# Kernel tuning notes

Hardware: AMD Instinct MI355X
Metric: run time of the kernel (lower is better)

Reference implementation:

```python
import jax, jax.numpy as jnp
import numpy as np
from jax import lax

N = 32768; L = 3000; PER_GRAPH = 64; NUM_GRAPHS = N // PER_GRAPH
DEG = 16; E = N * DEG
HID = 128; OUT3 = 64; NCLS = 2
RED = (L - 100) // 20 + 1   # 146
F_IN = 32 * RED             # 4672
EPS = 1e-5


def setup_inputs() -> dict:
    key = jax.random.key(0)
    ks = jax.random.split(key, 16)
    x = jax.random.normal(ks[0], (N, L), jnp.float32)
    # within-graph random edges: dst stays inside src's graph block
    src = jnp.repeat(jnp.arange(N, dtype=jnp.int32), DEG)
    dst = (src // PER_GRAPH) * PER_GRAPH + jax.random.randint(ks[1], (E,), 0, PER_GRAPH, dtype=jnp.int32)
    edge_index = jnp.stack([src, dst])
    edge_attr = jax.random.uniform(ks[2], (E,), jnp.float32, 0.1, 1.0)
    batch = jnp.repeat(jnp.arange(NUM_GRAPHS, dtype=jnp.int32), PER_GRAPH)
    g = lambda k, sh, fan: jax.random.normal(k, sh, jnp.float32) / np.float32(np.sqrt(fan))
    def bn(k, c):
        k1, k2 = jax.random.split(k)
        return (jnp.ones(c, jnp.float32), jnp.zeros(c, jnp.float32),
                0.1 * jax.random.normal(k1, (c,), jnp.float32),
                jax.random.uniform(k2, (c,), jnp.float32, 0.5, 1.5))
    g1, be1, m1, v1 = bn(ks[7], HID)
    g2, be2, m2, v2 = bn(ks[8], HID)
    g3, be3, m3, v3 = bn(ks[9], OUT3)
    return dict(x=x, edge_index=edge_index, edge_attr=edge_attr, batch=batch,
                conv_w=g(ks[3], (32, 1, 100), 100), conv_b=jnp.zeros(32, jnp.float32),
                W1=g(ks[4], (F_IN, HID), F_IN), b1=jnp.zeros(HID, jnp.float32),
                W2=g(ks[5], (HID, HID), HID), b2=jnp.zeros(HID, jnp.float32),
                W3=g(ks[6], (HID, OUT3), HID), b3=jnp.zeros(OUT3, jnp.float32),
                g1=g1, be1=be1, m1=m1, v1=v1,
                g2=g2, be2=be2, m2=m2, v2=v2,
                g3=g3, be3=be3, m3=m3, v3=v3,
                fc_w=g(ks[10], (OUT3, NCLS), OUT3), fc_b=jnp.zeros(NCLS, jnp.float32))


def _gcn(h, W, b, src, dst, w):
    # PyG GCNConv: linear (no bias) -> sym-normalized weighted aggregation with
    # self-loops (weight 1) -> + bias
    h = h @ W                                               # [N, C]
    deg = jax.ops.segment_sum(w, dst, num_segments=N) + 1.0  # + self-loop
    dinv = jnp.where(deg > 0, lax.rsqrt(deg), 0.0)
    norm = dinv[src] * w * dinv[dst]                         # [E]
    agg = jax.ops.segment_sum(h[src] * norm[:, None], dst, num_segments=N)
    return agg + h * (dinv * dinv)[:, None] + b              # self-loop term


def _bn(x, gamma, beta, mean, var):
    # eval-mode BatchNorm1d with running stats
    return (x - mean) * lax.rsqrt(var + EPS) * gamma + beta


def reference(x, edge_index, edge_attr, batch, conv_w, conv_b, W1, b1, W2, b2, W3, b3,
              g1, be1, m1, v1, g2, be2, m2, v2, g3, be3, m3, v3, fc_w, fc_b):
    src, dst = edge_index[0], edge_index[1]
    # Conv1d feature extractor: [N,1,L] -> [N,32,RED]
    h = lax.conv_general_dilated(x[:, None, :], conv_w, (20,), 'VALID',
                                 dimension_numbers=('NCH', 'OIH', 'NCH'))
    h = jax.nn.relu(h + conv_b[None, :, None]).reshape(N, F_IN)
    h = jax.nn.relu(_bn(_gcn(h, W1, b1, src, dst, edge_attr), g1, be1, m1, v1))
    h = jax.nn.relu(_bn(_gcn(h, W2, b2, src, dst, edge_attr), g2, be2, m2, v2))
    h = jax.nn.relu(_bn(_gcn(h, W3, b3, src, dst, edge_attr), g3, be3, m3, v3))
    # global mean pool over graphs
    sums = jax.ops.segment_sum(h, batch, num_segments=NUM_GRAPHS)
    cnt = jax.ops.segment_sum(jnp.ones((N,), h.dtype), batch, num_segments=NUM_GRAPHS)
    pooled = sums / cnt[:, None]
    return jax.nn.log_softmax(pooled @ fc_w + fc_b, axis=1)
```

## Files before the change

kernel.cpp:

```cpp
#include <hip/hip_runtime.h>
#include <math.h>

typedef float f32x4 __attribute__((ext_vector_type(4)));
typedef short bf16x8 __attribute__((ext_vector_type(8)));

constexpr int N_NODES = 32768;
constexpr int LEN     = 3000;
constexpr int HID     = 128;
constexpr int OUT3    = 64;
constexpr int E_TOT   = 32768*16;
constexpr int PG      = 64;
constexpr int EPG     = 1024;
constexpr int NG      = 512;
constexpr int NCHUNK  = 25;

__device__ __forceinline__ short bf1(float a) {
    unsigned u = __float_as_uint(a);
    return (short)((u + 0x7fff + ((u >> 16) & 1)) >> 16);
}
__device__ __forceinline__ unsigned bfpk2(float a, float b) {
    unsigned ua = __float_as_uint(a); ua = (ua + 0x7fff + ((ua >> 16) & 1)) >> 16;
    unsigned ub = __float_as_uint(b); ub = (ub + 0x7fff + ((ub >> 16) & 1)) >> 16;
    return (ua & 0xffffu) | (ub << 16);
}
__device__ __forceinline__ unsigned long long pk4(float a, float b, float c, float d) {
    return (unsigned long long)bfpk2(a, b) | ((unsigned long long)bfpk2(c, d) << 32);
}

__global__ void pack_w(const float* __restrict__ cw, short* __restrict__ wPf) {
    int tid = blockIdx.x * 256 + threadIdx.x;
    if (tid >= 512) return;
    int lane = tid & 63, i = tid >> 6;
    int Mt = i >> 2, ks = i & 3;
    int c  = Mt * 16 + (lane & 15);
    int kb = ks * 32 + (lane >> 4) * 8;
    bf16x8 v;
    #pragma unroll
    for (int j = 0; j < 8; j++) {
        int k = kb + j;
        v[j] = (k < 100) ? bf1(cw[c * 100 + k]) : (short)0;
    }
    *(bf16x8*)(wPf + tid * 8) = v;
}

__global__ void pack_w1(const float* __restrict__ W1, short* __restrict__ w1f) {
    int tid = blockIdx.x * 256 + threadIdx.x;
    if (tid >= 76800) return;
    int lane  = tid & 63;
    int rest  = tid >> 6;
    int ks    = rest % 6;
    int rest2 = rest / 6;
    int Nt    = rest2 & 7, chunk = rest2 >> 3;
    int r  = chunk * 6 + ks;
    int n  = Nt * 16 + (lane & 15);
    int cb = (lane >> 4) * 8;
    bf16x8 v;
    #pragma unroll
    for (int j = 0; j < 8; j++) {
        int c = cb + j;
        v[j] = (r < 146) ? bf1(W1[(c * 146 + r) * 128 + n]) : (short)0;
    }
    *(bf16x8*)(w1f + tid * 8) = v;
}

__global__ __launch_bounds__(256, 2) void conv_gemm1_mfma(
    const float* __restrict__ x, const short* __restrict__ wPf,
    const float* __restrict__ cbv, const short* __restrict__ w1f,
    float* __restrict__ z)
{
    __shared__ short xs[64 * 264];
    __shared__ short cbuf[64 * 196];

    const int t    = threadIdx.x;
    const int lane = t & 63;
    const int wv   = t >> 6;
    const int l15  = lane & 15;
    const int q    = lane >> 4;
    const int n0   = blockIdx.x * 64;

    bf16x8 wA[8];
    #pragma unroll
    for (int i = 0; i < 8; i++)
        wA[i] = *(const bf16x8*)(wPf + (i * 64 + lane) * 8);
    float cbr[8];
    #pragma unroll
    for (int i = 0; i < 8; i++)
        cbr[i] = cbv[(i >> 2) * 16 + q * 4 + (i & 3)];

    f32x4 acc[4][2];
    #pragma unroll
    for (int a = 0; a < 4; a++) { acc[a][0] = (f32x4)0.0f; acc[a][1] = (f32x4)0.0f; }

    const int NtG0 = wv * 2;
    const int NtC0 = wv * 6;

    #pragma unroll 1
    for (int c = 0; c < NCHUNK; c++) {
        const int r0 = c * 6;
        const int rcount = (146 - r0 < 6) ? (146 - r0) : 6;

        bf16x8 wB[12];
        #pragma unroll
        for (int u = 0; u < 12; u++) {
            int nt2 = u / 6, ks = u - nt2 * 6;
            int flat = (c * 8 + NtG0 + nt2) * 6 + ks;
            wB[u] = *(const bf16x8*)(w1f + (flat * 64 + lane) * 8);
        }

        __syncthreads();
        if (c == 0) {
            for (int u = t; u < 64 * 60; u += 256) {
                int node = u / 60, j = u - node * 60;
                int e = j * 4;
                const float4 vx = *(const float4*)&x[(size_t)(n0 + node) * LEN + e];
                *(unsigned long long*)&xs[node * 264 + (e & 255)] = pk4(vx.x, vx.y, vx.z, vx.w);
            }
        } else {
            const int L = 120 * c + 120;
            for (int u = t; u < 64 * 30; u += 256) {
                int node = u / 30, j = u - node * 30;
                int e  = L + j * 4;
                int ge = (e > 2996) ? 2996 : e;
                const float4 vx = *(const float4*)&x[(size_t)(n0 + node) * LEN + ge];
                *(unsigned long long*)&xs[node * 264 + (e & 255)] = pk4(vx.x, vx.y, vx.z, vx.w);
            }
        }
        __syncthreads();

        for (int ntc = 0; ntc < 6; ntc++) {
            int nn = (NtC0 + ntc) * 16 + l15;
            int m  = nn / 6;
            int rr = nn - m * 6;
            int eb = 20 * (r0 + rr) + q * 8;
            f32x4 ca0 = (f32x4)0.0f, ca1 = (f32x4)0.0f;
            #pragma unroll
            for (int ks = 0; ks < 4; ks++) {
                int e0 = eb + ks * 32;
                bf16x8 bx;
                ((unsigned long long*)&bx)[0] = *(const unsigned long long*)&xs[m * 264 + (e0 & 255)];
                ((unsigned long long*)&bx)[1] = *(const unsigned long long*)&xs[m * 264 + ((e0 + 4) & 255)];
                ca0 = __builtin_amdgcn_mfma_f32_16x16x32_bf16(wA[ks],     bx, ca0, 0, 0, 0);
                ca1 = __builtin_amdgcn_mfma_f32_16x16x32_bf16(wA[4 + ks], bx, ca1, 0, 0, 0);
            }
            const bool valid = (rr < rcount);
            const int wb = m * 196 + rr * 32 + q * 4;
            float v0 = valid ? fmaxf(ca0[0] + cbr[0], 0.f) : 0.f;
            float v1 = valid ? fmaxf(ca0[1] + cbr[1], 0.f) : 0.f;
            float v2 = valid ? fmaxf(ca0[2] + cbr[2], 0.f) : 0.f;
            float v3 = valid ? fmaxf(ca0[3] + cbr[3], 0.f) : 0.f;
            *(unsigned long long*)&cbuf[wb] = pk4(v0, v1, v2, v3);
            v0 = valid ? fmaxf(ca1[0] + cbr[4], 0.f) : 0.f;
            v1 = valid ? fmaxf(ca1[1] + cbr[5], 0.f) : 0.f;
            v2 = valid ? fmaxf(ca1[2] + cbr[6], 0.f) : 0.f;
            v3 = valid ? fmaxf(ca1[3] + cbr[7], 0.f) : 0.f;
            *(unsigned long long*)&cbuf[wb + 16] = pk4(v0, v1, v2, v3);
        }
        __syncthreads();

        #pragma unroll
        for (int ks = 0; ks < 6; ks++) {
            bf16x8 af[4];
            #pragma unroll
            for (int mt = 0; mt < 4; mt++) {
                int ad = (mt * 16 + l15) * 196 + ks * 32 + q * 8;
                ((unsigned long long*)&af[mt])[0] = *(const unsigned long long*)&cbuf[ad];
                ((unsigned long long*)&af[mt])[1] = *(const unsigned long long*)&cbuf[ad + 4];
            }
            #pragma unroll
            for (int mt = 0; mt < 4; mt++) {
                acc[mt][0] = __builtin_amdgcn_mfma_f32_16x16x32_bf16(af[mt], wB[ks],     acc[mt][0], 0, 0, 0);
                acc[mt][1] = __builtin_amdgcn_mfma_f32_16x16x32_bf16(af[mt], wB[6 + ks], acc[mt][1], 0, 0, 0);
            }
        }
    }

    #pragma unroll
    for (int mt = 0; mt < 4; mt++)
        #pragma unroll
        for (int nt2 = 0; nt2 < 2; nt2++)
            #pragma unroll
            for (int reg = 0; reg < 4; reg++) {
                int node = n0 + mt * 16 + q * 4 + reg;
                int f    = (NtG0 + nt2) * 16 + l15;
                z[(size_t)node * HID + f] = acc[mt][nt2][reg];
            }
}

__global__ __launch_bounds__(256) void graph_block(
    const float* __restrict__ z, const int* __restrict__ ei,
    const float* __restrict__ ew,
    const float* __restrict__ b1, const float* __restrict__ g1, const float* __restrict__ be1,
    const float* __restrict__ m1, const float* __restrict__ v1,
    const float* __restrict__ W2,
    const float* __restrict__ b2, const float* __restrict__ g2, const float* __restrict__ be2,
    const float* __restrict__ m2, const float* __restrict__ v2,
    const float* __restrict__ W3,
    const float* __restrict__ b3, const float* __restrict__ g3, const float* __restrict__ be3,
    const float* __restrict__ m3, const float* __restrict__ v3,
    const float* __restrict__ fcw, const float* __restrict__ fcb,
    float* __restrict__ out)
{
    __shared__ float At[64 * 68];
    __shared__ float buf[8704];
    __shared__ float dl[64];
    __shared__ float ps4[256];
    __shared__ float pooled[64];

    const int t  = threadIdx.x;
    const int g  = blockIdx.x;
    const int nb = g * PG;

    for (int i = t; i < 64 * 68; i += 256) At[i] = 0.f;
    if (t < 64) dl[t] = 0.f;
    __syncthreads();
    for (int i = t; i < EPG; i += 256) {
        int e = g * EPG + i;
        atomicAdd(&dl[ei[E_TOT + e] - nb], ew[e]);
    }
    __syncthreads();
    if (t < 64) dl[t] = rsqrtf(dl[t] + 1.0f);
    __syncthreads();
    for (int i = t; i < EPG; i += 256) {
        int e = g * EPG + i;
        int s = ei[e] - nb, d = ei[E_TOT + e] - nb;
        atomicAdd(&At[s * 68 + d], dl[s] * ew[e] * dl[d]);
    }
    if (t < 64) atomicAdd(&At[t * 68 + t], dl[t] * dl[t]);
    for (int i = t; i < 64 * HID; i += 256) buf[i] = z[(size_t)nb * HID + i];
    __syncthreads();

    const int f   = t & 127;
    const int ng  = t >> 7;
    const int n0  = ng * 32;
    const int f3  = t & 63;
    const int ng3 = t >> 6;
    const int n03 = ng3 * 16;

    float hreg[32];

#define LAYER128(BB, GG, BE, MM, VV)                                          \
    {                                                                         \
        float sc = GG[f] * rsqrtf(VV[f] + 1e-5f);                             \
        float mu = MM[f], bt = BE[f], bb = BB[f];                             \
        float a[32];                                                          \
        _Pragma("unroll")                                                     \
        for (int i = 0; i < 32; i++) a[i] = 0.f;                              \
        _Pragma("unroll 2")                                                   \
        for (int s = 0; s < 64; s++) {                                        \
            float zv = buf[s * 128 + f];                                      \
            _Pragma("unroll")                                                 \
            for (int qq = 0; qq < 8; qq++) {                                  \
                float4 a4 = *(const float4*)&At[s * 68 + n0 + qq * 4];        \
                a[qq*4+0] += a4.x * zv; a[qq*4+1] += a4.y * zv;               \
                a[qq*4+2] += a4.z * zv; a[qq*4+3] += a4.w * zv;               \
            }                                                                 \
        }                                                                     \
        _Pragma("unroll")                                                     \
        for (int i = 0; i < 32; i++)                                          \
            hreg[i] = fmaxf((a[i] + bb - mu) * sc + bt, 0.f);                 \
    }                                                                         \
    __syncthreads();                                                          \
    _Pragma("unroll")                                                         \
    for (int qq = 0; qq < 8; qq++)                                            \
        *(float4*)&buf[f * 68 + n0 + qq * 4] =                                \
            make_float4(hreg[qq*4], hreg[qq*4+1], hreg[qq*4+2], hreg[qq*4+3]);\
    __syncthreads();

#define GEMM128(WPTR)                                                         \
    {                                                                         \
        float a[32];                                                          \
        _Pragma("unroll")                                                     \
        for (int i = 0; i < 32; i++) a[i] = 0.f;                              \
        _Pragma("unroll 2")                                                   \
        for (int k = 0; k < 128; k++) {                                       \
            float wvv = WPTR[k * 128 + f];                                    \
            _Pragma("unroll")                                                 \
            for (int qq = 0; qq < 8; qq++) {                                  \
                float4 h4 = *(const float4*)&buf[k * 68 + n0 + qq * 4];       \
                a[qq*4+0] += h4.x * wvv; a[qq*4+1] += h4.y * wvv;             \
                a[qq*4+2] += h4.z * wvv; a[qq*4+3] += h4.w * wvv;             \
            }                                                                 \
        }                                                                     \
        __syncthreads();                                                      \
        _Pragma("unroll")                                                     \
        for (int i = 0; i < 32; i++) buf[(n0 + i) * 128 + f] = a[i];          \
        __syncthreads();                                                      \
    }

    LAYER128(b1, g1, be1, m1, v1)
    GEMM128(W2)
    LAYER128(b2, g2, be2, m2, v2)

    {
        float a[16];
        #pragma unroll
        for (int i = 0; i < 16; i++) a[i] = 0.f;
        #pragma unroll 2
        for (int k = 0; k < 128; k++) {
            float wvv = W3[k * 64 + f3];
            #pragma unroll
            for (int qq = 0; qq < 4; qq++) {
                float4 h4 = *(const float4*)&buf[k * 68 + n03 + qq * 4];
                a[qq*4+0] += h4.x * wvv; a[qq*4+1] += h4.y * wvv;
                a[qq*4+2] += h4.z * wvv; a[qq*4+3] += h4.w * wvv;
            }
        }
        __syncthreads();
        #pragma unroll
        for (int i = 0; i < 16; i++) buf[(n03 + i) * 64 + f3] = a[i];
        __syncthreads();
    }

    {
        float sc = g3[f3] * rsqrtf(v3[f3] + 1e-5f);
        float mu = m3[f3], bt = be3[f3], bb = b3[f3];
        float a[16];
        #pragma unroll
        for (int i = 0; i < 16; i++) a[i] = 0.f;
        #pragma unroll 2
        for (int s = 0; s < 64; s++) {
            float zv = buf[s * 64 + f3];
            #pragma unroll
            for (int qq = 0; qq < 4; qq++) {
                float4 a4 = *(const float4*)&At[s * 68 + n03 + qq * 4];
                a[qq*4+0] += a4.x * zv; a[qq*4+1] += a4.y * zv;
                a[qq*4+2] += a4.z * zv; a[qq*4+3] += a4.w * zv;
            }
        }
        float psum = 0.f;
        #pragma unroll
        for (int i = 0; i < 16; i++)
            psum += fmaxf((a[i] + bb - mu) * sc + bt, 0.f);
        ps4[ng3 * 64 + f3] = psum;
    }
    __syncthreads();
    if (t < 64) pooled[t] = (ps4[t] + ps4[64 + t] + ps4[128 + t] + ps4[192 + t]) * (1.f / 64.f);
    __syncthreads();
    if (t == 0) {
        float l0 = fcb[0], l1 = fcb[1];
        for (int ff = 0; ff < 64; ff++) { l0 += pooled[ff] * fcw[ff * 2]; l1 += pooled[ff] * fcw[ff * 2 + 1]; }
        float mx  = fmaxf(l0, l1);
        float lse = mx + logf(expf(l0 - mx) + expf(l1 - mx));
        out[g * 2 + 0] = l0 - lse;
        out[g * 2 + 1] = l1 - lse;
    }
#undef LAYER128
#undef GEMM128
}

extern "C" void kernel_launch(void* const* d_in, const int* in_sizes, int n_in,
                              void* d_out, int out_size, void* d_ws, size_t ws_size,
                              hipStream_t stream) {
    const float* x   = (const float*)d_in[0];
    const int*   ei  = (const int*)  d_in[1];
    const float* ew  = (const float*)d_in[2];
    const float* cw  = (const float*)d_in[4];
    const float* cb  = (const float*)d_in[5];
    const float* W1  = (const float*)d_in[6];
    const float* b1  = (const float*)d_in[7];
    const float* W2  = (const float*)d_in[8];
    const float* b2  = (const float*)d_in[9];
    const float* W3  = (const float*)d_in[10];
    const float* b3  = (const float*)d_in[11];
    const float* g1  = (const float*)d_in[12];
    const float* be1 = (const float*)d_in[13];
    const float* m1  = (const float*)d_in[14];
    const float* v1  = (const float*)d_in[15];
    const float* g2  = (const float*)d_in[16];
    const float* be2 = (const float*)d_in[17];
    const float* m2  = (const float*)d_in[18];
    const float* v2  = (const float*)d_in[19];
    const float* g3  = (const float*)d_in[20];
    const float* be3 = (const float*)d_in[21];
    const float* m3  = (const float*)d_in[22];
    const float* v3  = (const float*)d_in[23];
    const float* fcw = (const float*)d_in[24];
    const float* fcb = (const float*)d_in[25];
    float* out = (float*)d_out;

    float* z   = (float*)d_ws;
    short* wPf = (short*)((char*)d_ws + 16777216);
    short* w1f = (short*)((char*)d_ws + 16785408);

    pack_w  <<<2,   256, 0, stream>>>(cw, wPf);
    pack_w1 <<<300, 256, 0, stream>>>(W1, w1f);
    conv_gemm1_mfma<<<NG, 256, 0, stream>>>(x, wPf, cb, w1f, z);
    graph_block<<<NG, 256, 0, stream>>>(z, ei, ew,
        b1, g1, be1, m1, v1, W2,
        b2, g2, be2, m2, v2, W3,
        b3, g3, be3, m3, v3, fcw, fcb, out);
}
```

Baseline: 753.2 us.

## Prefetch next x chunk into registers and restructure conv stage per-node ownership

The x-window load is reorganised so each thread owns a fixed node row. The next chunk's float4 values are prefetched into registers before the barrier and written to the shared ring buffer after the conv MFMA stage. This removes one __syncthreads per chunk and overlaps global loads with compute. The conv stage now has each wave handle 16 fixed nodes across 6 rows instead of the div/mod mapping, and bf16 packing switches to cheaper round-half-up rounding. The cost is more register pressure (13 and then 8 float4 held live) and slightly different rounding.

Result: faster. 686.1 us (-8.9%).

```diff
diff --git a/kernel.cpp b/kernel.cpp
--- a/kernel.cpp
+++ b/kernel.cpp
@@ -3,6 +3,8 @@
 
 typedef float f32x4 __attribute__((ext_vector_type(4)));
 typedef short bf16x8 __attribute__((ext_vector_type(8)));
+typedef unsigned int u32;
+typedef unsigned long long u64;
 
 constexpr int N_NODES = 32768;
 constexpr int LEN     = 3000;
@@ -13,18 +15,17 @@
 constexpr int EPG     = 1024;
 constexpr int NG      = 512;
 constexpr int NCHUNK  = 25;
+constexpr int XS_S    = 260;
+constexpr int CBS     = 196;
 
 __device__ __forceinline__ short bf1(float a) {
     unsigned u = __float_as_uint(a);
     return (short)((u + 0x7fff + ((u >> 16) & 1)) >> 16);
 }
-__device__ __forceinline__ unsigned bfpk2(float a, float b) {
-    unsigned ua = __float_as_uint(a); ua = (ua + 0x7fff + ((ua >> 16) & 1)) >> 16;
-    unsigned ub = __float_as_uint(b); ub = (ub + 0x7fff + ((ub >> 16) & 1)) >> 16;
-    return (ua & 0xffffu) | (ub << 16);
-}
-__device__ __forceinline__ unsigned long long pk4(float a, float b, float c, float d) {
-    return (unsigned long long)bfpk2(a, b) | ((unsigned long long)bfpk2(c, d) << 32);
+__device__ __forceinline__ u32 pk2(float lo, float hi) {
+    u32 ua = __float_as_uint(lo) + 0x8000u;
+    u32 ub = __float_as_uint(hi) + 0x8000u;
+    return (ua >> 16) | (ub & 0xffff0000u);
 }
 
 __global__ void pack_w(const float* __restrict__ cw, short* __restrict__ wPf) {
@@ -68,15 +69,18 @@
     const float* __restrict__ cbv, const short* __restrict__ w1f,
     float* __restrict__ z)
 {
-    __shared__ short xs[64 * 264];
-    __shared__ short cbuf[64 * 196];
-
-    const int t    = threadIdx.x;
-    const int lane = t & 63;
-    const int wv   = t >> 6;
-    const int l15  = lane & 15;
-    const int q    = lane >> 4;
-    const int n0   = blockIdx.x * 64;
+    __shared__ short xs[64 * XS_S];
+    __shared__ short cbuf[64 * CBS];
+
+    const int t     = threadIdx.x;
+    const int lane  = t & 63;
+    const int wv    = t >> 6;
+    const int l15   = lane & 15;
+    const int q     = lane >> 4;
+    const int n0    = blockIdx.x * 64;
+    const int j4    = lane & 3;
+    const int nodeS = wv * 16 + (lane >> 2);
+    const int nodeC = wv * 16 + l15;
 
     bf16x8 wA[8];
     #pragma unroll
@@ -92,69 +96,80 @@
     for (int a = 0; a < 4; a++) { acc[a][0] = (f32x4)0.0f; acc[a][1] = (f32x4)0.0f; }
 
     const int NtG0 = wv * 2;
-    const int NtC0 = wv * 6;
+    const float* xpS = x + (size_t)(n0 + nodeS) * LEN;
+    short* xrow = xs + nodeS * XS_S;
+
+    {
+        float4 v[13];
+        #pragma unroll
+        for (int it = 0; it < 13; it++)
+            v[it] = *(const float4*)(xpS + (j4 + 4 * it) * 4);
+        #pragma unroll
+        for (int it = 0; it < 13; it++) {
+            int e = (j4 + 4 * it) * 4;
+            *(uint2*)&xrow[e] = make_uint2(pk2(v[it].x, v[it].y), pk2(v[it].z, v[it].w));
+        }
+    }
 
     #pragma unroll 1
     for (int c = 0; c < NCHUNK; c++) {
         const int r0 = c * 6;
         const int rcount = (146 - r0 < 6) ? (146 - r0) : 6;
 
+        float4 xn[8];
+        if (c < NCHUNK - 1) {
+            const int ebase = 120 * c + 200;
+            #pragma unroll
+            for (int it = 0; it < 8; it++) {
+                int e  = ebase + (j4 + 4 * it) * 4;
+                int ge = e > 2996 ? 2996 : e;
+                xn[it] = *(const float4*)(xpS + ge);
+            }
+        }
         bf16x8 wB[12];
         #pragma unroll
-        for (int u = 0; u < 12; u++) {
-            int nt2 = u / 6, ks = u - nt2 * 6;
-            int flat = (c * 8 + NtG0 + nt2) * 6 + ks;
-            wB[u] = *(const bf16x8*)(w1f + (flat * 64 + lane) * 8);
-        }
+        for (int u = 0; u < 12; u++)
+            wB[u] = *(const bf16x8*)(w1f + ((c * 48 + NtG0 * 6 + u) * 64 + lane) * 8);
 
         __syncthreads();
-        if (c == 0) {
-            for (int u = t; u < 64 * 60; u += 256) {
-                int node = u / 60, j = u - node * 60;
-                int e = j * 4;
-                const float4 vx = *(const float4*)&x[(size_t)(n0 + node) * LEN + e];
-                *(unsigned long long*)&xs[node * 264 + (e & 255)] = pk4(vx.x, vx.y, vx.z, vx.w);
-            }
-        } else {
-            const int L = 120 * c + 120;
-            for (int u = t; u < 64 * 30; u += 256) {
-                int node = u / 30, j = u - node * 30;
-                int e  = L + j * 4;
-                int ge = (e > 2996) ? 2996 : e;
-                const float4 vx = *(const float4*)&x[(size_t)(n0 + node) * LEN + ge];
-                *(unsigned long long*)&xs[node * 264 + (e & 255)] = pk4(vx.x, vx.y, vx.z, vx.w);
-            }
-        }
-        __syncthreads();
-
-        for (int ntc = 0; ntc < 6; ntc++) {
-            int nn = (NtC0 + ntc) * 16 + l15;
-            int m  = nn / 6;
-            int rr = nn - m * 6;
-            int eb = 20 * (r0 + rr) + q * 8;
+
+        const short* xr = xs + nodeC * XS_S;
+        #pragma unroll
+        for (int rr = 0; rr < 6; rr++) {
+            const int eb = 20 * (r0 + rr) + 8 * q;
             f32x4 ca0 = (f32x4)0.0f, ca1 = (f32x4)0.0f;
             #pragma unroll
             for (int ks = 0; ks < 4; ks++) {
-                int e0 = eb + ks * 32;
+                int e0 = eb + 32 * ks;
                 bf16x8 bx;
-                ((unsigned long long*)&bx)[0] = *(const unsigned long long*)&xs[m * 264 + (e0 & 255)];
-                ((unsigned long long*)&bx)[1] = *(const unsigned long long*)&xs[m * 264 + ((e0 + 4) & 255)];
+                *(u64*)&bx       = *(const u64*)&xr[e0 & 255];
+                *((u64*)&bx + 1) = *(const u64*)&xr[(e0 + 4) & 255];
                 ca0 = __builtin_amdgcn_mfma_f32_16x16x32_bf16(wA[ks],     bx, ca0, 0, 0, 0);
                 ca1 = __builtin_amdgcn_mfma_f32_16x16x32_bf16(wA[4 + ks], bx, ca1, 0, 0, 0);
             }
-            const bool valid = (rr < rcount);
-            const int wb = m * 196 + rr * 32 + q * 4;
-            float v0 = valid ? fmaxf(ca0[0] + cbr[0], 0.f) : 0.f;
-            float v1 = valid ? fmaxf(ca0[1] + cbr[1], 0.f) : 0.f;
-            float v2 = valid ? fmaxf(ca0[2] + cbr[2], 0.f) : 0.f;
-            float v3 = valid ? fmaxf(ca0[3] + cbr[3], 0.f) : 0.f;
-            *(unsigned long long*)&cbuf[wb] = pk4(v0, v1, v2, v3);
-            v0 = valid ? fmaxf(ca1[0] + cbr[4], 0.f) : 0.f;
-            v1 = valid ? fmaxf(ca1[1] + cbr[5], 0.f) : 0.f;
-            v2 = valid ? fmaxf(ca1[2] + cbr[6], 0.f) : 0.f;
-            v3 = valid ? fmaxf(ca1[3] + cbr[7], 0.f) : 0.f;
-            *(unsigned long long*)&cbuf[wb + 16] = pk4(v0, v1, v2, v3);
-        }
+            short* cw_ = cbuf + nodeC * CBS + rr * 32 + q * 4;
+            if (rr < rcount) {
+                u32 p0 = pk2(fmaxf(ca0[0] + cbr[0], 0.f), fmaxf(ca0[1] + cbr[1], 0.f));
+                u32 p1 = pk2(fmaxf(ca0[2] + cbr[2], 0.f), fmaxf(ca0[3] + cbr[3], 0.f));
+                *(uint2*)cw_ = make_uint2(p0, p1);
+                p0 = pk2(fmaxf(ca1[0] + cbr[4], 0.f), fmaxf(ca1[1] + cbr[5], 0.f));
+                p1 = pk2(fmaxf(ca1[2] + cbr[6], 0.f), fmaxf(ca1[3] + cbr[7], 0.f));
+                *(uint2*)(cw_ + 16) = make_uint2(p0, p1);
+            } else {
+                *(uint2*)cw_        = make_uint2(0u, 0u);
+                *(uint2*)(cw_ + 16) = make_uint2(0u, 0u);
+            }
+        }
+
+        if (c < NCHUNK - 1) {
+            const int ebase = 120 * c + 200;
+            #pragma unroll
+            for (int it = 0; it < 8; it++) {
+                int e = ebase + (j4 + 4 * it) * 4;
+                *(uint2*)&xrow[e & 255] = make_uint2(pk2(xn[it].x, xn[it].y), pk2(xn[it].z, xn[it].w));
+            }
+        }
+
         __syncthreads();
 
         #pragma unroll
@@ -162,9 +177,9 @@
             bf16x8 af[4];
             #pragma unroll
             for (int mt = 0; mt < 4; mt++) {
-                int ad = (mt * 16 + l15) * 196 + ks * 32 + q * 8;
-                ((unsigned long long*)&af[mt])[0] = *(const unsigned long long*)&cbuf[ad];
-                ((unsigned long long*)&af[mt])[1] = *(const unsigned long long*)&cbuf[ad + 4];
+                const short* ap = cbuf + (mt * 16 + l15) * CBS + ks * 32 + q * 8;
+                *(u64*)&af[mt]       = *(const u64*)ap;
+                *((u64*)&af[mt] + 1) = *(const u64*)(ap + 4);
             }
             #pragma unroll
             for (int mt = 0; mt < 4; mt++) {
```
